# Kernel optimization log

Measured on AMD Instinct MI355X. Metric: run time of the kernel, lower is better.

Reference implementation:

```python
import jax, jax.numpy as jnp
import numpy as np

COST_CLASS = 1.0
COST_OBJECTNESS = 5.0
COST_GIOU = 2.0
COST_CENTER = 10.0

B, Q, G, C = 32, 1024, 64, 256


def _lsa(cost):
    """Exact rectangular linear sum assignment (Jonker-Volgenant shortest
    augmenting path, same algorithm as scipy.optimize.linear_sum_assignment).
    cost: (R, Cc) float64 numpy array. Returns (row_ind, col_ind), row_ind sorted."""
    transposed = cost.shape[0] > cost.shape[1]
    if transposed:
        cost = cost.T
    n, m = cost.shape
    u = np.zeros(n)
    v = np.zeros(m)
    col4row = np.full(n, -1, dtype=np.int64)
    row4col = np.full(m, -1, dtype=np.int64)
    for cur_row in range(n):
        shortest = np.full(m, np.inf)
        path = np.full(m, -1, dtype=np.int64)
        SC = np.zeros(m, dtype=bool)
        SR_rows = []
        min_val = 0.0
        i = cur_row
        sink = -1
        while sink == -1:
            SR_rows.append(i)
            idx = np.where(~SC)[0]
            r = min_val + cost[i, idx] - u[i] - v[idx]
            better = r < shortest[idx]
            upd = idx[better]
            shortest[upd] = r[better]
            path[upd] = i
            j = idx[np.argmin(shortest[idx])]
            min_val = shortest[j]
            SC[j] = True
            if row4col[j] == -1:
                sink = j
            else:
                i = row4col[j]
        # dual variable update
        u[cur_row] += min_val
        for irow in SR_rows:
            if irow != cur_row:
                u[irow] += min_val - shortest[col4row[irow]]
        v[SC] -= min_val - shortest[SC]
        # augment along the alternating path back to cur_row
        j = sink
        while True:
            i = path[j]
            row4col[j] = i
            col4row[i], j = j, col4row[i]
            if i == cur_row:
                break
    if transposed:
        order = np.argsort(col4row)
        return col4row[order], np.arange(n)[order]
    return np.arange(n), col4row


def setup_inputs() -> dict:
    key = jax.random.key(0)
    k1, k2, k3, k4, k5 = jax.random.split(key, 5)
    return {
        "sem_cls_prob": jax.random.uniform(k1, (B, Q, C), dtype=jnp.float32),
        "objectness_prob": jax.random.uniform(k2, (B, Q), dtype=jnp.float32),
        "center_dist": jax.random.uniform(k3, (B, Q, G), dtype=jnp.float32),
        "gious": jax.random.uniform(k4, (B, Q, G), dtype=jnp.float32),
        "nactual_gt": jax.random.randint(k5, (B,), 0, G, dtype=jnp.int64)
        if jax.config.jax_enable_x64 else jax.random.randint(k5, (B,), 0, G).astype(jnp.int32),
    }


def reference(sem_cls_prob, objectness_prob, center_dist, gious, nactual_gt):
    batchsize, nprop = objectness_prob.shape
    # class_mat == 0 in the original module
    final_cost = (COST_OBJECTNESS * (-objectness_prob[..., None])
                  + COST_CENTER * center_dist
                  + COST_GIOU * (-gious))  # [B, Q, G]
    cost_np = np.asarray(final_cost, dtype=np.float64)
    ngt = np.asarray(nactual_gt)
    per_prop_gt_inds = np.zeros((batchsize, nprop), dtype=np.int64)
    proposal_matched_mask = np.zeros((batchsize, nprop), dtype=np.float32)
    for b in range(batchsize):  # per-batch independent Hungarian (as in source)
        g = int(ngt[b])
        if g > 0:
            rows, cols = _lsa(cost_np[b, :, :g])
            per_prop_gt_inds[b, rows] = cols
            proposal_matched_mask[b, rows] = 1.0
    return jnp.asarray(per_prop_gt_inds), jnp.asarray(proposal_matched_mask)
```

## Files before the change

kernel.cpp:

```cpp
#include <hip/hip_runtime.h>
#include <math.h>

#define B_ 32
#define Q_ 1024
#define G_ 64
#define K16 16

template<int CTRL>
__device__ __forceinline__ double dpp_f64(double x) {
    union { double d; int i[2]; } a; a.d = x;
    union { int i[2]; double d; } r;
    r.i[0] = __builtin_amdgcn_update_dpp(a.i[0], a.i[0], CTRL, 0xF, 0xF, false);
    r.i[1] = __builtin_amdgcn_update_dpp(a.i[1], a.i[1], CTRL, 0xF, 0xF, false);
    return r.d;
}
template<int CTRL>
__device__ __forceinline__ float dpp_f32(float x) {
    union { float f; int i; } a; a.f = x;
    union { int i; float f; } r;
    r.i = __builtin_amdgcn_update_dpp(a.i, a.i, CTRL, 0xF, 0xF, false);
    return r.f;
}
#define ROR1 0x121
#define ROR2 0x122
#define ROR4 0x124
#define ROR8 0x128
#define BC15 0x142
#define BC31 0x143

__device__ __forceinline__ double readlane_f64(double x, int sl) {
    const int s = __builtin_amdgcn_readfirstlane(sl);
    union { double d; int i2[2]; } a; a.d = x;
    union { int i2[2]; double d; } r;
    r.i2[0] = __builtin_amdgcn_readlane(a.i2[0], s);
    r.i2[1] = __builtin_amdgcn_readlane(a.i2[1], s);
    return r.d;
}
__device__ __forceinline__ float readlane_f32u(float x, int sl) {
    union { float f; int i; } a; a.f = x;
    union { int i; float f; } r;
    r.i = __builtin_amdgcn_readlane(a.i, __builtin_amdgcn_readfirstlane(sl));
    return r.f;
}
__device__ __forceinline__ float readlane_f32c(float x, int sl) {
    union { float f; int i; } a; a.f = x;
    union { int i; float f; } r;
    r.i = __builtin_amdgcn_readlane(a.i, sl);
    return r.f;
}
__device__ __forceinline__ int readlane_i32(int x, int sl) {
    return __builtin_amdgcn_readlane(x, __builtin_amdgcn_readfirstlane(sl));
}
__device__ __forceinline__ int sel16(const int* p, int s) {
    int v = p[0];
    #pragma unroll
    for (int k = 1; k < K16; ++k) v = (s == k) ? p[k] : v;
    return v;
}

__global__ __launch_bounds__(256) void build_kernel(
    const float* __restrict__ obj, const float* __restrict__ cd,
    const float* __restrict__ gi, float* __restrict__ ct,
    float* __restrict__ pv, int* __restrict__ pj)
{
    __shared__ float tile[64][65];
    const int b  = blockIdx.y;
    const int jb = blockIdx.x << 6;
    const int t  = threadIdx.x;
    const float* objb = obj + (b << 10);
    const float4* cd4 = (const float4*)(cd + ((size_t)b << 16));
    const float4* gi4 = (const float4*)(gi + ((size_t)b << 16));

    #pragma unroll
    for (int p = 0; p < 4; ++p) {
        const int f  = t + (p << 8);
        const int jj = f >> 4;
        const int q  = f & 15;
        const int i0 = q << 2;
        const int j  = jb + jj;
        const float om = __fmul_rn(5.0f, -objb[j]);
        const float4 c4 = cd4[(j << 4) + q];
        const float4 q4 = gi4[(j << 4) + q];
        tile[i0 + 0][jj] = __fadd_rn(__fadd_rn(om, __fmul_rn(10.0f, c4.x)), __fmul_rn(2.0f, -q4.x));
        tile[i0 + 1][jj] = __fadd_rn(__fadd_rn(om, __fmul_rn(10.0f, c4.y)), __fmul_rn(2.0f, -q4.y));
        tile[i0 + 2][jj] = __fadd_rn(__fadd_rn(om, __fmul_rn(10.0f, c4.z)), __fmul_rn(2.0f, -q4.z));
        tile[i0 + 3][jj] = __fadd_rn(__fadd_rn(om, __fmul_rn(10.0f, c4.w)), __fmul_rn(2.0f, -q4.w));
    }
    __syncthreads();
    #pragma unroll
    for (int r = 0; r < 16; ++r) {
        const int idx = (r << 8) + t;
        const int i = idx >> 6, j2 = idx & 63;
        ct[(((size_t)(b << 6) + i) << 10) + jb + j2] = tile[i][j2];
    }
    if (t < 64) {
        float bv = tile[t][0]; int bc = 0;
        #pragma unroll 8
        for (int c = 1; c < 64; ++c) {
            const float v = tile[t][c];
            if (v < bv) { bv = v; bc = c; }
        }
        const int o = (((b << 6) + t) << 4) + blockIdx.x;
        pv[o] = bv;
        pj[o] = jb + bc;
    }
}

template<bool HASWS>
__global__ __launch_bounds__(64) void matcher_k(
    const float* __restrict__ obj, const float* __restrict__ cd,
    const float* __restrict__ gi, const int* __restrict__ ngt,
    const float* __restrict__ ct, const float* __restrict__ pv,
    const int* __restrict__ pj, float* __restrict__ out_ind,
    float* __restrict__ out_mask)
{
    __shared__ int    row4col_[Q_];
    __shared__ double sh_lds[Q_];

    const int b = blockIdx.x;
    const int l = threadIdx.x;
    const int g = ngt[b];

    for (int j = l; j < Q_; j += 64) row4col_[j] = -1;
    __builtin_amdgcn_wave_barrier();

    const float* objb = obj + (b << 10);
    const float* cdb  = cd + ((size_t)b << 16);
    const float* gib  = gi + ((size_t)b << 16);
    const float* ctb  = HASWS ? (ct + ((size_t)(b << 6) << 10)) : (const float*)nullptr;

    float objm[K16];
    if (!HASWS) {
        #pragma unroll
        for (int k = 0; k < K16; ++k) objm[k] = __fmul_rn(5.0f, -objb[l + (k << 6)]);
    }
    auto load_row = [&](int i, float* c) {
        if (HASWS) {
            #pragma unroll
            for (int k = 0; k < K16; ++k) c[k] = ctb[((size_t)i << 10) + l + (k << 6)];
        } else {
            #pragma unroll
            for (int k = 0; k < K16; ++k) {
                const int j = l + (k << 6);
                const int idx = (j << 6) + i;
                c[k] = __fadd_rn(__fadd_rn(objm[k], __fmul_rn(10.0f, cdb[idx])),
                                 __fmul_rn(2.0f, -gib[idx]));
            }
        }
    };

    float pre_v = 0.0f; int pre_j = 0;
    if (HASWS) {
        const float* pvb = pv + (((b << 6) + l) << 4);
        const int*   pjb = pj + (((b << 6) + l) << 4);
        float bv = pvb[0]; int bj = pjb[0];
        #pragma unroll
        for (int q = 1; q < 16; ++q) {
            const float v = pvb[q];
            const int  j = pjb[q];
            if (v < bv) { bv = v; bj = j; }
        }
        pre_v = bv; pre_j = bj;
    } else if (g > 0) {
        for (int i = 0; i < g; ++i) {
            float c[K16];
            load_row(i, c);
            float t8[8];
            #pragma unroll
            for (int m = 0; m < 8; ++m) t8[m] = fminf(c[2 * m], c[2 * m + 1]);
            float bv = fminf(fminf(fminf(t8[0], t8[1]), fminf(t8[2], t8[3])),
                             fminf(fminf(t8[4], t8[5]), fminf(t8[6], t8[7])));
            bv = fminf(bv, dpp_f32<ROR1>(bv));
            bv = fminf(bv, dpp_f32<ROR2>(bv));
            bv = fminf(bv, dpp_f32<ROR4>(bv));
            bv = fminf(bv, dpp_f32<ROR8>(bv));
            bv = fminf(bv, dpp_f32<BC15>(bv));
            bv = fminf(bv, dpp_f32<BC31>(bv));
            const float gv = readlane_f32c(bv, 63);
            unsigned long long mk[K16];
            #pragma unroll
            for (int k = 0; k < K16; ++k) mk[k] = __ballot(c[k] == gv);
            int j0 = 0;
            #pragma unroll
            for (int k = K16 - 1; k >= 0; --k)
                if (mk[k]) j0 = (k << 6) | (int)__builtin_ctzll(mk[k]);
            pre_v = (l == i) ? gv : pre_v;
            pre_j = (l == i) ? j0 : pre_j;
        }
    }

    auto lexmin64 = [&](const double* cand, double& gv_o, int& jm_o) {
        double t8[8];
        #pragma unroll
        for (int m = 0; m < 8; ++m) t8[m] = fmin(cand[2 * m], cand[2 * m + 1]);
        const double a4 = fmin(fmin(t8[0], t8[1]), fmin(t8[2], t8[3]));
        const double b4 = fmin(fmin(t8[4], t8[5]), fmin(t8[6], t8[7]));
        double bv = fmin(a4, b4);
        bv = fmin(bv, dpp_f64<ROR1>(bv));
        bv = fmin(bv, dpp_f64<ROR2>(bv));
        bv = fmin(bv, dpp_f64<ROR4>(bv));
        bv = fmin(bv, dpp_f64<ROR8>(bv));
        bv = fmin(bv, dpp_f64<BC15>(bv));
        bv = fmin(bv, dpp_f64<BC31>(bv));
        const double gv = readlane_f64(bv, 63);
        unsigned long long mk[K16];
        #pragma unroll
        for (int k = 0; k < K16; ++k) mk[k] = __ballot(cand[k] == gv);
        int jm = 0;
        #pragma unroll
        for (int k = K16 - 1; k >= 0; --k)
            if (mk[k]) jm = (k << 6) | (int)__builtin_ctzll(mk[k]);
        gv_o = gv; jm_o = jm;
    };

    const double INF = __builtin_inf();
    double u_rep   = 0.0;
    int    c4r_rep = -1;
    unsigned asg   = 0u;
    unsigned dirty = 0u;
    double v_r[K16], sh_r[K16];
    int    path_r[K16];
    float  c_row[K16];
    #pragma unroll
    for (int k = 0; k < K16; ++k) { v_r[k] = 0.0; path_r[k] = 0; }

    for (int cur = 0; cur < g; ++cur) {
        double minv = (double)readlane_f32u(pre_v, cur);
        int jm = readlane_i32(pre_j, cur);
        const unsigned dw = (unsigned)readlane_i32((int)dirty, jm & 63);
        if ((dw >> (jm >> 6)) & 1u) {
            load_row(cur, c_row);
            double r[K16];
            #pragma unroll
            for (int k = 0; k < K16; ++k) r[k] = (double)c_row[k] - v_r[k];
            lexmin64(r, minv, jm);
        }
        const int owner0 = jm & 63, slot0 = jm >> 6;
        const unsigned oa0 = (unsigned)readlane_i32((int)asg, owner0);

        if (!((oa0 >> slot0) & 1u)) {
            u_rep   = (l == cur)    ? u_rep + minv : u_rep;
            c4r_rep = (l == cur)    ? jm           : c4r_rep;
            asg     = (l == owner0) ? (asg | (1u << slot0)) : asg;
            if (l == 0) row4col_[jm] = cur;
            __builtin_amdgcn_wave_barrier();
        } else {
            load_row(cur, c_row);
            unsigned sc = 0u;
            #pragma unroll
            for (int k = 0; k < K16; ++k) {
                sh_r[k] = (double)c_row[k] - v_r[k];
                path_r[k] = cur;
            }
            if (l == owner0) sc |= 1u << slot0;
            int i = row4col_[jm];
            bool inSR = (l == cur) || (l == i);
            double ui = readlane_f64(u_rep, i);
            load_row(i, c_row);
            int sink = -1;

            while (sink < 0) {
                double cand[K16];
                #pragma unroll
                for (int k = 0; k < K16; ++k) {
                    const double rr = ((minv + (double)c_row[k]) - ui) - v_r[k];
                    const bool notSC = !((sc >> k) & 1u);
                    const bool upd = notSC && (rr < sh_r[k]);
                    sh_r[k]   = upd ? rr : sh_r[k];
                    path_r[k] = upd ? i : path_r[k];
                    cand[k] = notSC ? sh_r[k] : INF;
                }
                lexmin64(cand, minv, jm);
                if (l == (jm & 63)) sc |= 1u << (jm >> 6);
                const unsigned oa = (unsigned)readlane_i32((int)asg, jm & 63);
                if (!((oa >> (jm >> 6)) & 1u)) {
                    sink = jm;
                } else {
                    i = row4col_[jm];
                    if (l == i) inSR = true;
                    ui = readlane_f64(u_rep, i);
                    load_row(i, c_row);
                }
            }

            if (l == cur) u_rep += minv;
            #pragma unroll
            for (int k = 0; k < K16; ++k) sh_lds[l + (k << 6)] = sh_r[k];
            __builtin_amdgcn_wave_barrier();
            if (inSR && l != cur) u_rep += minv - sh_lds[c4r_rep];
            __builtin_amdgcn_wave_barrier();
            #pragma unroll
            for (int k = 0; k < K16; ++k) {
                const double nv = v_r[k] - (minv - sh_r[k]);
                v_r[k] = ((sc >> k) & 1u) ? nv : v_r[k];
            }
            dirty |= sc;

            int j = sink;
            while (true) {
                const int so = j & 63, ss = j >> 6;
                const int ii = readlane_i32(sel16(path_r, ss), so);
                const int nj = readlane_i32(c4r_rep, ii);
                if (l == 0) row4col_[j] = ii;
                if (l == so) asg |= 1u << ss;
                if (l == ii) c4r_rep = j;
                j = nj;
                if (ii == cur) break;
            }
            __builtin_amdgcn_wave_barrier();
        }
    }

    __builtin_amdgcn_wave_barrier();
    for (int j = l; j < Q_; j += 64) {
        const int rc = row4col_[j];
        out_ind [(b << 10) + j] = (rc >= 0) ? (float)rc : 0.0f;
        out_mask[(b << 10) + j] = (rc >= 0) ? 1.0f : 0.0f;
    }
}

extern "C" void kernel_launch(void* const* d_in, const int* in_sizes, int n_in,
                              void* d_out, int out_size, void* d_ws, size_t ws_size,
                              hipStream_t stream)
{
    const float* obj = (const float*)d_in[1];
    const float* cd  = (const float*)d_in[2];
    const float* gi  = (const float*)d_in[3];
    const int*   ngt = (const int*)d_in[4];
    float* out0 = (float*)d_out;
    float* out1 = out0 + B_ * Q_;

    const size_t ct_b = (size_t)B_ * G_ * Q_ * sizeof(float);
    const size_t pv_b = (size_t)B_ * G_ * 16 * sizeof(float);
    if (ws_size >= ct_b + 2 * pv_b) {
        float* ct = (float*)d_ws;
        float* pv = (float*)((char*)d_ws + ct_b);
        int*   pj = (int*)((char*)d_ws + ct_b + pv_b);
        build_kernel<<<dim3(16, B_), 256, 0, stream>>>(obj, cd, gi, ct, pv, pj);
        matcher_k<true><<<B_, 64, 0, stream>>>(obj, cd, gi, ngt, ct, pv, pj, out0, out1);
    } else {
        matcher_k<false><<<B_, 64, 0, stream>>>(obj, cd, gi, ngt,
                                                nullptr, nullptr, nullptr, out0, out1);
    }
}
```

Before: 169.1 us.

## Keep row4col in registers and fuse argmin with index via DPP pair reduction

Moves the row4col array and the shortest-path buffer out of LDS into per-lane registers, reading entries with a tree select plus readlane. Dual updates now use a recorded min value per row instead of a scatter through LDS. The min reduction carries value and index together through DPP steps, replacing 16 ballots and a ctz scan. The change also sets launch bounds to one block per unit, and the extra registers and select trees may add VGPR pressure and ALU work on the serial augmenting path.

```diff
diff --git a/kernel.cpp b/kernel.cpp
--- a/kernel.cpp
+++ b/kernel.cpp
@@ -5,6 +5,13 @@
 #define Q_ 1024
 #define G_ 64
 #define K16 16
+
+#define ROR1 0x121
+#define ROR2 0x122
+#define ROR4 0x124
+#define ROR8 0x128
+#define BC15 0x142
+#define BC31 0x143
 
 template<int CTRL>
 __device__ __forceinline__ double dpp_f64(double x) {
@@ -15,18 +22,9 @@
     return r.d;
 }
 template<int CTRL>
-__device__ __forceinline__ float dpp_f32(float x) {
-    union { float f; int i; } a; a.f = x;
-    union { int i; float f; } r;
-    r.i = __builtin_amdgcn_update_dpp(a.i, a.i, CTRL, 0xF, 0xF, false);
-    return r.f;
-}
-#define ROR1 0x121
-#define ROR2 0x122
-#define ROR4 0x124
-#define ROR8 0x128
-#define BC15 0x142
-#define BC31 0x143
+__device__ __forceinline__ int dpp_i32(int x) {
+    return __builtin_amdgcn_update_dpp(x, x, CTRL, 0xF, 0xF, false);
+}
 
 __device__ __forceinline__ double readlane_f64(double x, int sl) {
     const int s = __builtin_amdgcn_readfirstlane(sl);
@@ -36,26 +34,55 @@
     r.i2[1] = __builtin_amdgcn_readlane(a.i2[1], s);
     return r.d;
 }
+__device__ __forceinline__ double readlane_f64c(double x, int sl) {
+    union { double d; int i2[2]; } a; a.d = x;
+    union { int i2[2]; double d; } r;
+    r.i2[0] = __builtin_amdgcn_readlane(a.i2[0], sl);
+    r.i2[1] = __builtin_amdgcn_readlane(a.i2[1], sl);
+    return r.d;
+}
 __device__ __forceinline__ float readlane_f32u(float x, int sl) {
     union { float f; int i; } a; a.f = x;
     union { int i; float f; } r;
     r.i = __builtin_amdgcn_readlane(a.i, __builtin_amdgcn_readfirstlane(sl));
     return r.f;
 }
-__device__ __forceinline__ float readlane_f32c(float x, int sl) {
-    union { float f; int i; } a; a.f = x;
-    union { int i; float f; } r;
-    r.i = __builtin_amdgcn_readlane(a.i, sl);
-    return r.f;
-}
 __device__ __forceinline__ int readlane_i32(int x, int sl) {
     return __builtin_amdgcn_readlane(x, __builtin_amdgcn_readfirstlane(sl));
 }
-__device__ __forceinline__ int sel16(const int* p, int s) {
-    int v = p[0];
-    #pragma unroll
-    for (int k = 1; k < K16; ++k) v = (s == k) ? p[k] : v;
-    return v;
+__device__ __forceinline__ int readlane_i32c(int x, int sl) {
+    return __builtin_amdgcn_readlane(x, sl);
+}
+
+__device__ __forceinline__ int sel16t(const int* p, int s) {
+    int t0[8];
+    #pragma unroll
+    for (int m = 0; m < 8; ++m) t0[m] = (s & 1) ? p[2*m+1] : p[2*m];
+    int t1[4];
+    #pragma unroll
+    for (int m = 0; m < 4; ++m) t1[m] = (s & 2) ? t0[2*m+1] : t0[2*m];
+    const int a0 = (s & 4) ? t1[1] : t1[0];
+    const int a1 = (s & 4) ? t1[3] : t1[2];
+    return (s & 8) ? a1 : a0;
+}
+
+__device__ __forceinline__ void lexpair(const double* cand, int l,
+                                        double& gv_o, int& jm_o) {
+    double v = cand[0]; int j = l;
+    #pragma unroll
+    for (int k = 1; k < K16; ++k) {
+        const bool t = cand[k] < v;
+        v = t ? cand[k] : v;
+        j = t ? (l + (k << 6)) : j;
+    }
+#define LP_STEP(C) { const double pv = dpp_f64<C>(v); const int pj = dpp_i32<C>(j); \
+    const bool t = (pv < v) || ((pv == v) && (pj < j)); \
+    v = t ? pv : v; j = t ? pj : j; }
+    LP_STEP(ROR1) LP_STEP(ROR2) LP_STEP(ROR4) LP_STEP(ROR8)
+    LP_STEP(BC15) LP_STEP(BC31)
+#undef LP_STEP
+    gv_o = readlane_f64c(v, 63);
+    jm_o = readlane_i32c(j, 63);
 }
 
 __global__ __launch_bounds__(256) void build_kernel(
@@ -107,22 +134,16 @@
 }
 
 template<bool HASWS>
-__global__ __launch_bounds__(64) void matcher_k(
+__global__ __launch_bounds__(64, 1) void matcher_k(
     const float* __restrict__ obj, const float* __restrict__ cd,
     const float* __restrict__ gi, const int* __restrict__ ngt,
     const float* __restrict__ ct, const float* __restrict__ pv,
     const int* __restrict__ pj, float* __restrict__ out_ind,
     float* __restrict__ out_mask)
 {
-    __shared__ int    row4col_[Q_];
-    __shared__ double sh_lds[Q_];
-
     const int b = blockIdx.x;
     const int l = threadIdx.x;
     const int g = ngt[b];
-
-    for (int j = l; j < Q_; j += 64) row4col_[j] = -1;
-    __builtin_amdgcn_wave_barrier();
 
     const float* objb = obj + (b << 10);
     const float* cdb  = cd + ((size_t)b << 16);
@@ -141,8 +162,8 @@
         } else {
             #pragma unroll
             for (int k = 0; k < K16; ++k) {
-                const int j = l + (k << 6);
-                const int idx = (j << 6) + i;
+                const int jj = l + (k << 6);
+                const int idx = (jj << 6) + i;
                 c[k] = __fadd_rn(__fadd_rn(objm[k], __fmul_rn(10.0f, cdb[idx])),
                                  __fmul_rn(2.0f, -gib[idx]));
             }
@@ -156,84 +177,48 @@
         float bv = pvb[0]; int bj = pjb[0];
         #pragma unroll
         for (int q = 1; q < 16; ++q) {
-            const float v = pvb[q];
-            const int  j = pjb[q];
-            if (v < bv) { bv = v; bj = j; }
+            const float vq = pvb[q];
+            const int  jq = pjb[q];
+            if (vq < bv) { bv = vq; bj = jq; }
         }
         pre_v = bv; pre_j = bj;
     } else if (g > 0) {
         for (int i = 0; i < g; ++i) {
-            float c[K16];
-            load_row(i, c);
-            float t8[8];
-            #pragma unroll
-            for (int m = 0; m < 8; ++m) t8[m] = fminf(c[2 * m], c[2 * m + 1]);
-            float bv = fminf(fminf(fminf(t8[0], t8[1]), fminf(t8[2], t8[3])),
-                             fminf(fminf(t8[4], t8[5]), fminf(t8[6], t8[7])));
-            bv = fminf(bv, dpp_f32<ROR1>(bv));
-            bv = fminf(bv, dpp_f32<ROR2>(bv));
-            bv = fminf(bv, dpp_f32<ROR4>(bv));
-            bv = fminf(bv, dpp_f32<ROR8>(bv));
-            bv = fminf(bv, dpp_f32<BC15>(bv));
-            bv = fminf(bv, dpp_f32<BC31>(bv));
-            const float gv = readlane_f32c(bv, 63);
-            unsigned long long mk[K16];
-            #pragma unroll
-            for (int k = 0; k < K16; ++k) mk[k] = __ballot(c[k] == gv);
-            int j0 = 0;
-            #pragma unroll
-            for (int k = K16 - 1; k >= 0; --k)
-                if (mk[k]) j0 = (k << 6) | (int)__builtin_ctzll(mk[k]);
-            pre_v = (l == i) ? gv : pre_v;
+            float c[K16]; load_row(i, c);
+            double c64[K16];
+            #pragma unroll
+            for (int k = 0; k < K16; ++k) c64[k] = (double)c[k];
+            double gv; int j0;
+            lexpair(c64, l, gv, j0);
+            pre_v = (l == i) ? (float)gv : pre_v;
             pre_j = (l == i) ? j0 : pre_j;
         }
     }
 
-    auto lexmin64 = [&](const double* cand, double& gv_o, int& jm_o) {
-        double t8[8];
-        #pragma unroll
-        for (int m = 0; m < 8; ++m) t8[m] = fmin(cand[2 * m], cand[2 * m + 1]);
-        const double a4 = fmin(fmin(t8[0], t8[1]), fmin(t8[2], t8[3]));
-        const double b4 = fmin(fmin(t8[4], t8[5]), fmin(t8[6], t8[7]));
-        double bv = fmin(a4, b4);
-        bv = fmin(bv, dpp_f64<ROR1>(bv));
-        bv = fmin(bv, dpp_f64<ROR2>(bv));
-        bv = fmin(bv, dpp_f64<ROR4>(bv));
-        bv = fmin(bv, dpp_f64<ROR8>(bv));
-        bv = fmin(bv, dpp_f64<BC15>(bv));
-        bv = fmin(bv, dpp_f64<BC31>(bv));
-        const double gv = readlane_f64(bv, 63);
-        unsigned long long mk[K16];
-        #pragma unroll
-        for (int k = 0; k < K16; ++k) mk[k] = __ballot(cand[k] == gv);
-        int jm = 0;
-        #pragma unroll
-        for (int k = K16 - 1; k >= 0; --k)
-            if (mk[k]) jm = (k << 6) | (int)__builtin_ctzll(mk[k]);
-        gv_o = gv; jm_o = jm;
-    };
-
     const double INF = __builtin_inf();
-    double u_rep   = 0.0;
+    double u_rep = 0.0;
+    double m_rec = 0.0;
+    bool   inSR  = false;
     int    c4r_rep = -1;
     unsigned asg   = 0u;
     unsigned dirty = 0u;
     double v_r[K16], sh_r[K16];
-    int    path_r[K16];
-    float  c_row[K16];
-    #pragma unroll
-    for (int k = 0; k < K16; ++k) { v_r[k] = 0.0; path_r[k] = 0; }
+    int    path_r[K16], r4c_r[K16];
+    float  c_cur[K16], c_i[K16];
+    #pragma unroll
+    for (int k = 0; k < K16; ++k) { v_r[k] = 0.0; path_r[k] = 0; r4c_r[k] = -1; }
 
     for (int cur = 0; cur < g; ++cur) {
         double minv = (double)readlane_f32u(pre_v, cur);
         int jm = readlane_i32(pre_j, cur);
         const unsigned dw = (unsigned)readlane_i32((int)dirty, jm & 63);
+        bool have_cur = false;
         if ((dw >> (jm >> 6)) & 1u) {
-            load_row(cur, c_row);
-            double r[K16];
-            #pragma unroll
-            for (int k = 0; k < K16; ++k) r[k] = (double)c_row[k] - v_r[k];
-            lexmin64(r, minv, jm);
+            load_row(cur, c_cur); have_cur = true;
+            double rr0[K16];
+            #pragma unroll
+            for (int k = 0; k < K16; ++k) rr0[k] = (double)c_cur[k] - v_r[k];
+            lexpair(rr0, l, minv, jm);
         }
         const int owner0 = jm & 63, slot0 = jm >> 6;
         const unsigned oa0 = (unsigned)readlane_i32((int)asg, owner0);
@@ -242,53 +227,52 @@
             u_rep   = (l == cur)    ? u_rep + minv : u_rep;
             c4r_rep = (l == cur)    ? jm           : c4r_rep;
             asg     = (l == owner0) ? (asg | (1u << slot0)) : asg;
-            if (l == 0) row4col_[jm] = cur;
-            __builtin_amdgcn_wave_barrier();
+            #pragma unroll
+            for (int k = 0; k < K16; ++k)
+                r4c_r[k] = (l == owner0 && k == slot0) ? cur : r4c_r[k];
         } else {
-            load_row(cur, c_row);
-            unsigned sc = 0u;
+            if (!have_cur) load_row(cur, c_cur);
+            int i = readlane_i32(sel16t(r4c_r, slot0), owner0);
+            double ui = readlane_f64(u_rep, i);
+            load_row(i, c_i);
+            unsigned sc = (l == owner0) ? (1u << slot0) : 0u;
+            inSR  = (l == i);
+            m_rec = minv;
             #pragma unroll
             for (int k = 0; k < K16; ++k) {
-                sh_r[k] = (double)c_row[k] - v_r[k];
+                sh_r[k] = (double)c_cur[k] - v_r[k];
                 path_r[k] = cur;
             }
-            if (l == owner0) sc |= 1u << slot0;
-            int i = row4col_[jm];
-            bool inSR = (l == cur) || (l == i);
-            double ui = readlane_f64(u_rep, i);
-            load_row(i, c_row);
+
             int sink = -1;
-
             while (sink < 0) {
                 double cand[K16];
                 #pragma unroll
                 for (int k = 0; k < K16; ++k) {
-                    const double rr = ((minv + (double)c_row[k]) - ui) - v_r[k];
+                    const double rr = ((minv + (double)c_i[k]) - ui) - v_r[k];
                     const bool notSC = !((sc >> k) & 1u);
                     const bool upd = notSC && (rr < sh_r[k]);
                     sh_r[k]   = upd ? rr : sh_r[k];
                     path_r[k] = upd ? i : path_r[k];
                     cand[k] = notSC ? sh_r[k] : INF;
                 }
-                lexmin64(cand, minv, jm);
-                if (l == (jm & 63)) sc |= 1u << (jm >> 6);
-                const unsigned oa = (unsigned)readlane_i32((int)asg, jm & 63);
-                if (!((oa >> (jm >> 6)) & 1u)) {
+                lexpair(cand, l, minv, jm);
+                const int ow = jm & 63, sl = jm >> 6;
+                if (l == ow) sc |= (1u << sl);
+                const int insp = readlane_i32(sel16t(r4c_r, sl), ow);
+                const unsigned oa = (unsigned)readlane_i32((int)asg, ow);
+                if (!((oa >> sl) & 1u)) {
                     sink = jm;
                 } else {
-                    i = row4col_[jm];
-                    if (l == i) inSR = true;
+                    i = insp;
+                    if (l == i) { inSR = true; m_rec = minv; }
                     ui = readlane_f64(u_rep, i);
-                    load_row(i, c_row);
+                    load_row(i, c_i);
                 }
             }
 
-            if (l == cur) u_rep += minv;
-            #pragma unroll
-            for (int k = 0; k < K16; ++k) sh_lds[l + (k << 6)] = sh_r[k];
-            __builtin_amdgcn_wave_barrier();
-            if (inSR && l != cur) u_rep += minv - sh_lds[c4r_rep];
-            __builtin_amdgcn_wave_barrier();
+            if (l == cur)       u_rep += minv;
+            else if (inSR)      u_rep += minv - m_rec;
             #pragma unroll
             for (int k = 0; k < K16; ++k) {
                 const double nv = v_r[k] - (minv - sh_r[k]);
@@ -299,23 +283,25 @@
             int j = sink;
             while (true) {
                 const int so = j & 63, ss = j >> 6;
-                const int ii = readlane_i32(sel16(path_r, ss), so);
+                const int ii = readlane_i32(sel16t(path_r, ss), so);
                 const int nj = readlane_i32(c4r_rep, ii);
-                if (l == 0) row4col_[j] = ii;
-                if (l == so) asg |= 1u << ss;
-                if (l == ii) c4r_rep = j;
+                #pragma unroll
+                for (int k = 0; k < K16; ++k)
+                    r4c_r[k] = (l == so && k == ss) ? ii : r4c_r[k];
+                asg     = (l == so) ? (asg | (1u << ss)) : asg;
+                c4r_rep = (l == ii) ? j : c4r_rep;
                 j = nj;
                 if (ii == cur) break;
             }
-            __builtin_amdgcn_wave_barrier();
-        }
-    }
-
-    __builtin_amdgcn_wave_barrier();
-    for (int j = l; j < Q_; j += 64) {
-        const int rc = row4col_[j];
-        out_ind [(b << 10) + j] = (rc >= 0) ? (float)rc : 0.0f;
-        out_mask[(b << 10) + j] = (rc >= 0) ? 1.0f : 0.0f;
+        }
+    }
+
+    #pragma unroll
+    for (int k = 0; k < K16; ++k) {
+        const int rc = r4c_r[k];
+        const int jj = l + (k << 6);
+        out_ind [(b << 10) + jj] = (rc >= 0) ? (float)rc : 0.0f;
+        out_mask[(b << 10) + jj] = (rc >= 0) ? 1.0f : 0.0f;
     }
 }
 
```

Result: slower. 205.7 us (+21.6%).
